# Kernel tuning notes

Hardware: AMD Instinct MI355X
Metric: run time of the kernel (lower is better)

## Reference

```python
import jax, jax.numpy as jnp
import numpy as np

FACTOR = 1  # init factor -> top_k = int(factor * log(L))


def setup_inputs() -> dict:
    key = jax.random.key(0)
    kq, kk, kv = jax.random.split(key, 3)
    B, L, H, E = 16, 2048, 8, 64
    shape = (B, L, H, E)
    return {
        "queries": jax.random.normal(kq, shape, dtype=jnp.float32),
        "keys": jax.random.normal(kk, shape, dtype=jnp.float32),
        "values": jax.random.normal(kv, shape, dtype=jnp.float32),
    }


def reference(queries, keys, values):
    B, L, H, E = queries.shape
    # seq lens equal -> torch's pad/truncate branch is a no-op slice
    q = jnp.transpose(queries, (0, 2, 3, 1))  # [B,H,E,L]
    k = jnp.transpose(keys, (0, 2, 3, 1))
    v = jnp.transpose(values, (0, 2, 3, 1))

    # FFT-based circular cross-correlation along time
    qf = jnp.fft.rfft(q, axis=-1)
    kf = jnp.fft.rfft(k, axis=-1)
    corr = jnp.fft.irfft(qf * jnp.conj(kf), n=L, axis=-1)  # [B,H,E,L]

    top_k = int(FACTOR * np.log(L))  # static: 7 for L=2048
    mean_value = corr.mean(axis=(1, 2))  # mean over head then variates -> [B,L]
    # global (batch-averaged) top-k delays, shared across batch (training path)
    _, topk_index = jax.lax.top_k(mean_value.mean(axis=0), top_k)  # [k]
    # per-batch weights at those delays, softmax over k
    w = jax.nn.softmax(mean_value[:, topk_index], axis=-1)  # [B,k]

    # torch.roll(v, -d, -1)[..., t] == v[..., (t + d) % L]
    idx = (jnp.arange(L)[None, :] + topk_index[:, None]) % L  # [k,L]
    gathered = v[..., idx]  # [B,H,E,k,L]
    agg = jnp.einsum('bhekl,bk->bhel', gathered, w)  # weighted delay aggregation

    return jnp.transpose(agg, (0, 3, 1, 2))  # back to [B,L,H,E]
```

## Files before the change

kernel.cpp:

```cpp
#include <hip/hip_runtime.h>
#include <hip/hip_bf16.h>
#include <math.h>


#define B_ 16
#define L_ 2048
#define H_ 8
#define E_ 64
#define C_ (H_ * E_)
#define NCH (B_ * C_)
#define K_ 7

#define PART_OFF 0ull
#define SG_OFF   33554432ull
#define MV_OFF   (SG_OFF + 2097152ull)
#define TK_OFF   (MV_OFF + 131072ull)
#define W_OFF    (TK_OFF + 64ull)

__device__ __forceinline__ float2 cadd(float2 a, float2 b) { return make_float2(a.x + b.x, a.y + b.y); }
__device__ __forceinline__ float2 csub(float2 a, float2 b) { return make_float2(a.x - b.x, a.y - b.y); }
__device__ __forceinline__ float2 cmul(float2 a, float2 b) {
  return make_float2(fmaf(a.x, b.x, -a.y * b.y), fmaf(a.x, b.y, a.y * b.x));
}
__device__ __forceinline__ float2 cis(float ang) { float s, c; sincosf(ang, &s, &c); return make_float2(c, s); }

template<int S> __device__ __forceinline__ float2 rot90(float2 z) {
  return (S < 0) ? make_float2(z.y, -z.x) : make_float2(-z.y, z.x);
}
template<int S> __device__ __forceinline__ void dft4(float2& a, float2& b, float2& c, float2& d) {
  float2 t0 = cadd(a, c), t1 = csub(a, c), t2 = cadd(b, d), t3 = rot90<S>(csub(b, d));
  a = cadd(t0, t2); c = csub(t0, t2); b = cadd(t1, t3); d = csub(t1, t3);
}
template<int S> __device__ __forceinline__ void dft8(float2 v[8]) {
  const float RT = 0.70710678118654752f;
  const float SR = (S < 0) ? -RT : RT;
  float2 a0 = cadd(v[0], v[4]), a1 = cadd(v[1], v[5]), a2 = cadd(v[2], v[6]), a3 = cadd(v[3], v[7]);
  float2 b0 = csub(v[0], v[4]), b1 = csub(v[1], v[5]), b2 = csub(v[2], v[6]), b3 = csub(v[3], v[7]);
  b1 = cmul(b1, make_float2(RT, SR));
  b2 = rot90<S>(b2);
  b3 = cmul(b3, make_float2(-RT, SR));
  dft4<S>(a0, a1, a2, a3);
  dft4<S>(b0, b1, b2, b3);
  v[0] = a0; v[2] = a1; v[4] = a2; v[6] = a3;
  v[1] = b0; v[3] = b1; v[5] = b2; v[7] = b3;
}
__device__ __forceinline__ int sg(int e) { return e + (e >> 5); }

__global__ __launch_bounds__(256) void fft_corr_kernel(
    const float* __restrict__ q, const float* __restrict__ k,
    float2* __restrict__ part) {
  extern __shared__ float2 dbuf[];
  int t = threadIdx.x;
  int j2 = t & 31, j3 = t & 3;
  float2 tw1[7], tw2[7], tw3[7];
  {
    float2 w1 = cis(-6.283185307179586f * (float)t  / 2048.0f);
    float2 w2 = cis(-6.283185307179586f * (float)j2 / 256.0f);
    float2 w3 = cis(-6.283185307179586f * (float)j3 / 32.0f);
    tw1[0] = w1; tw2[0] = w2; tw3[0] = w3;
#pragma unroll
    for (int kk = 1; kk < 7; ++kk) {
      tw1[kk] = cmul(tw1[kk - 1], w1);
      tw2[kk] = cmul(tw2[kk - 1], w2);
      tw3[kk] = cmul(tw3[kk - 1], w3);
    }
  }
  int pphys = blockIdx.x;
  int i = pphys >> 3, x = pphys & 7;
  int l = ((i >> 2) << 5) | (x << 2) | (i & 3);
  int cbase = l * 4;
  int b = cbase >> 9, h = (cbase >> 6) & 7, e0 = cbase & 63;
  size_t base = (size_t)b * (L_ * H_ * E_) + (size_t)h * E_ + e0;

  float4 qv[8], kv[8];
#pragma unroll
  for (int m = 0; m < 8; ++m) {
    size_t a = base + (size_t)(t + 256 * m) * (H_ * E_);
    qv[m] = *(const float4*)(q + a);
    kv[m] = *(const float4*)(k + a);
  }

  float2 acc[8];
#pragma unroll
  for (int kk = 0; kk < 8; ++kk) acc[kk] = make_float2(0.f, 0.f);

#pragma unroll
  for (int c = 0; c < 4; ++c) {
    float2 v[8];
#pragma unroll
    for (int m = 0; m < 8; ++m)
      v[m] = make_float2(((const float*)&qv[m])[c], ((const float*)&kv[m])[c]);
    dft8<-1>(v);
#pragma unroll
    for (int kk = 1; kk < 8; ++kk) v[kk] = cmul(v[kk], tw1[kk - 1]);
    float2* bufc = dbuf + c * 2112;
#pragma unroll
    for (int kk = 0; kk < 8; ++kk) bufc[sg(t + 256 * kk)] = v[kk];
  }
  __syncthreads();

  int base2 = (t >> 5) * 256 + j2;
  int base3 = (t >> 2) * 32 + j3;
#pragma unroll
  for (int cp = 0; cp < 2; ++cp) {
    float2* A  = dbuf + (2 * cp) * 2112;
    float2* Bf = dbuf + (2 * cp + 1) * 2112;
    float2 va[8], vb[8];
#pragma unroll
    for (int m = 0; m < 8; ++m) { va[m] = A[sg(base2 + 32 * m)]; vb[m] = Bf[sg(base2 + 32 * m)]; }
    dft8<-1>(va); dft8<-1>(vb);
#pragma unroll
    for (int kk = 1; kk < 8; ++kk) { va[kk] = cmul(va[kk], tw2[kk - 1]); vb[kk] = cmul(vb[kk], tw2[kk - 1]); }
#pragma unroll
    for (int kk = 0; kk < 8; ++kk) { A[sg(base2 + 32 * kk)] = va[kk]; Bf[sg(base2 + 32 * kk)] = vb[kk]; }
    __syncthreads();
#pragma unroll
    for (int m = 0; m < 8; ++m) { va[m] = A[sg(base3 + 4 * m)]; vb[m] = Bf[sg(base3 + 4 * m)]; }
    dft8<-1>(va); dft8<-1>(vb);
#pragma unroll
    for (int kk = 1; kk < 8; ++kk) { va[kk] = cmul(va[kk], tw3[kk - 1]); vb[kk] = cmul(vb[kk], tw3[kk - 1]); }
#pragma unroll
    for (int kk = 0; kk < 8; ++kk) { A[sg(base3 + 4 * kk)] = va[kk]; Bf[sg(base3 + 4 * kk)] = vb[kk]; }
    __syncthreads();
#pragma unroll
    for (int kk = 0; kk < 8; ++kk) { va[kk] = A[sg(8 * t + kk)]; vb[kk] = Bf[sg(8 * t + kk)]; }
    dft4<-1>(va[0], va[1], va[2], va[3]); dft4<-1>(va[4], va[5], va[6], va[7]);
    dft4<-1>(vb[0], vb[1], vb[2], vb[3]); dft4<-1>(vb[4], vb[5], vb[6], vb[7]);
#pragma unroll
    for (int kk = 0; kk < 8; ++kk) { A[sg(8 * t + kk)] = va[kk]; Bf[sg(8 * t + kk)] = vb[kk]; }
    __syncthreads();
#pragma unroll
    for (int kk = 0; kk < 8; ++kk) {
      int pos = 8 * t + kk;
      int f  = ((pos >> 8) & 7) | (((pos >> 5) & 7) << 3) | (((pos >> 2) & 7) << 6) | ((pos & 3) << 9);
      int fp = (2048 - f) & 2047;
      int pp = ((fp & 7) << 8) | (((fp >> 3) & 7) << 5) | (((fp >> 6) & 7) << 2) | ((fp >> 9) & 3);
      float2 Ax = va[kk], Bc = A[sg(pp)];
      acc[kk].x += 0.5f  * (Bc.x * Ax.y + Bc.y * Ax.x);
      acc[kk].y += 0.25f * (Ax.x * Ax.x + Ax.y * Ax.y - Bc.x * Bc.x - Bc.y * Bc.y);
      Ax = vb[kk]; Bc = Bf[sg(pp)];
      acc[kk].x += 0.5f  * (Bc.x * Ax.y + Bc.y * Ax.x);
      acc[kk].y += 0.25f * (Ax.x * Ax.x + Ax.y * Ax.y - Bc.x * Bc.x - Bc.y * Bc.y);
    }
  }
#pragma unroll
  for (int kk = 0; kk < 8; ++kk) dbuf[sg(8 * t + kk)] = acc[kk];
  __syncthreads();
  float2* prow = part + (size_t)l * L_;
#pragma unroll
  for (int m = 0; m < 8; ++m) prow[t + 256 * m] = dbuf[sg(t + 256 * m)];
}

__global__ __launch_bounds__(256) void reduce_R_kernel(
    const float2* __restrict__ part, float2* __restrict__ Sg) {
  int idx = blockIdx.x * 256 + threadIdx.x;
  int p = idx & 2047;
  int g = (idx >> 11) & 7;
  int b = idx >> 14;
  float2 s = make_float2(0.f, 0.f);
#pragma unroll 4
  for (int i = 0; i < 16; ++i) {
    float2 vv = part[(size_t)(b * 128 + g * 16 + i) * L_ + p];
    s.x += vv.x; s.y += vv.y;
  }
  Sg[idx] = s;
}

__global__ __launch_bounds__(256) void ifft_kernel(
    const float2* __restrict__ Sg, float* __restrict__ mv) {
  __shared__ float2 buf[2112];
  int t = threadIdx.x, b = blockIdx.x;
  int j2 = t & 31, j3 = t & 3;
  float2 tw1[7], tw2[7], tw3[7];
  {
    float2 w1 = cis(6.283185307179586f * (float)t  / 2048.0f);
    float2 w2 = cis(6.283185307179586f * (float)j2 / 256.0f);
    float2 w3 = cis(6.283185307179586f * (float)j3 / 32.0f);
    tw1[0] = w1; tw2[0] = w2; tw3[0] = w3;
#pragma unroll
    for (int kk = 1; kk < 7; ++kk) {
      tw1[kk] = cmul(tw1[kk - 1], w1);
      tw2[kk] = cmul(tw2[kk - 1], w2);
      tw3[kk] = cmul(tw3[kk - 1], w3);
    }
  }
  int base2 = (t >> 5) * 256 + j2;
  int base3 = (t >> 2) * 32 + j3;
  float2 u[8];
#pragma unroll
  for (int kk = 0; kk < 8; ++kk) u[kk] = make_float2(0.f, 0.f);
#pragma unroll
  for (int g = 0; g < 8; ++g) {
    const float4* rp = (const float4*)(Sg + (size_t)(b * 8 + g) * L_);
#pragma unroll
    for (int m = 0; m < 4; ++m) {
      float4 f = rp[4 * t + m];
      u[2 * m].x     += f.x; u[2 * m].y     += f.y;
      u[2 * m + 1].x += f.z; u[2 * m + 1].y += f.w;
    }
  }
  dft4<1>(u[0], u[1], u[2], u[3]);
  dft4<1>(u[4], u[5], u[6], u[7]);
#pragma unroll
  for (int kk = 0; kk < 8; ++kk) buf[sg(8 * t + kk)] = u[kk];
  __syncthreads();
  float2 v[8];
#pragma unroll
  for (int kk = 0; kk < 8; ++kk) v[kk] = buf[sg(base3 + 4 * kk)];
#pragma unroll
  for (int kk = 1; kk < 8; ++kk) v[kk] = cmul(v[kk], tw3[kk - 1]);
  dft8<1>(v);
  __syncthreads();
#pragma unroll
  for (int m = 0; m < 8; ++m) buf[sg(base3 + 4 * m)] = v[m];
  __syncthreads();
#pragma unroll
  for (int kk = 0; kk < 8; ++kk) v[kk] = buf[sg(base2 + 32 * kk)];
#pragma unroll
  for (int kk = 1; kk < 8; ++kk) v[kk] = cmul(v[kk], tw2[kk - 1]);
  dft8<1>(v);
  __syncthreads();
#pragma unroll
  for (int m = 0; m < 8; ++m) buf[sg(base2 + 32 * m)] = v[m];
  __syncthreads();
#pragma unroll
  for (int kk = 0; kk < 8; ++kk) v[kk] = buf[sg(t + 256 * kk)];
#pragma unroll
  for (int kk = 1; kk < 8; ++kk) v[kk] = cmul(v[kk], tw1[kk - 1]);
  dft8<1>(v);
  const float scale = 1.0f / (2048.0f * 512.0f);
#pragma unroll
  for (int m = 0; m < 8; ++m) mv[b * L_ + t + 256 * m] = v[m].x * scale;
}

__global__ __launch_bounds__(256) void topk_kernel(
    const float* __restrict__ mv, int* __restrict__ topk, float* __restrict__ wts) {
  __shared__ float av[2048];
  __shared__ float rv[256];
  __shared__ int   ri[256];
  __shared__ int   sidx[K_];
  int tid = threadIdx.x;
  for (int d = tid; d < 2048; d += 256) {
    float s = 0.f;
#pragma unroll
    for (int b = 0; b < B_; ++b) s += mv[b * L_ + d];
    av[d] = s;
  }
  __syncthreads();
  for (int kk = 0; kk < K_; ++kk) {
    float bv = -INFINITY; int bi = 0;
    for (int d = tid; d < 2048; d += 256) {
      float vv = av[d];
      if (vv > bv) { bv = vv; bi = d; }
    }
    rv[tid] = bv; ri[tid] = bi;
    __syncthreads();
    for (int off = 128; off > 0; off >>= 1) {
      if (tid < off) {
        float v2 = rv[tid + off]; int i2 = ri[tid + off];
        if (v2 > rv[tid] || (v2 == rv[tid] && i2 < ri[tid])) { rv[tid] = v2; ri[tid] = i2; }
      }
      __syncthreads();
    }
    if (tid == 0) { sidx[kk] = ri[0]; av[ri[0]] = -INFINITY; }
    __syncthreads();
  }
  if (tid < K_) topk[tid] = sidx[tid];
  if (tid < B_) {
    float xk[K_], m = -INFINITY;
#pragma unroll
    for (int kk = 0; kk < K_; ++kk) { xk[kk] = mv[tid * L_ + sidx[kk]]; m = fmaxf(m, xk[kk]); }
    float s = 0.f;
#pragma unroll
    for (int kk = 0; kk < K_; ++kk) { xk[kk] = expf(xk[kk] - m); s += xk[kk]; }
#pragma unroll
    for (int kk = 0; kk < K_; ++kk) wts[tid * K_ + kk] = xk[kk] / s;
  }
}

__global__ __launch_bounds__(256) void aggregate_kernel(
    const float4* __restrict__ v4, const int* __restrict__ topk,
    const float* __restrict__ wts, float4* __restrict__ out4) {
  __shared__ int   sidx[K_];
  __shared__ float sw[B_][K_];
  int tid = threadIdx.x;
  if (tid < K_) sidx[tid] = topk[tid];
  if (tid < B_ * K_) sw[tid / K_][tid % K_] = wts[tid];
  __syncthreads();
  int idx = blockIdx.x * 256 + tid;
  int c4  = idx & 127;
  int row = idx >> 7;
  int t   = row & (L_ - 1);
  int b   = row >> 11;
  float4 acc = make_float4(0.f, 0.f, 0.f, 0.f);
#pragma unroll
  for (int kk = 0; kk < K_; ++kk) {
    int s = t + sidx[kk];
    if (s >= L_) s -= L_;
    float w = sw[b][kk];
    float4 val = v4[((size_t)(b * L_ + s) << 7) + c4];
    acc.x += w * val.x; acc.y += w * val.y;
    acc.z += w * val.z; acc.w += w * val.w;
  }
  out4[idx] = acc;
}

extern "C" void kernel_launch(void* const* d_in, const int* in_sizes, int n_in,
                              void* d_out, int out_size, void* d_ws, size_t ws_size,
                              hipStream_t stream) {
  const float* q = (const float*)d_in[0];
  const float* k = (const float*)d_in[1];
  const float* v = (const float*)d_in[2];
  float* out = (float*)d_out;

  char* ws = (char*)d_ws;
  float2* part = (float2*)(ws + PART_OFF);
  float2* Sg   = (float2*)(ws + SG_OFF);
  float*  mv   = (float*) (ws + MV_OFF);
  int*    topk = (int*)   (ws + TK_OFF);
  float*  wts  = (float*) (ws + W_OFF);

  fft_corr_kernel<<<NCH / 4, 256, 4 * 2112 * sizeof(float2), stream>>>(q, k, part);
  reduce_R_kernel<<<(B_ * 8 * L_) / 256, 256, 0, stream>>>(part, Sg);
  ifft_kernel<<<B_, 256, 0, stream>>>(Sg, mv);
  topk_kernel<<<1, 256, 0, stream>>>(mv, topk, wts);
  aggregate_kernel<<<(B_ * L_ * C_ / 4) / 256, 256, 0, stream>>>(
      (const float4*)v, topk, wts, (float4*)out);
}
```

Before: 156.9 us.

## Process two channels per FFT block instead of four to cut LDS and registers

The FFT correlation kernel now handles 2 channels per block (float2 loads) instead of 4, halving shared memory per block and register usage, and doubling the block count. The partial-sum buffer grows to twice as many rows, so the reduce kernel sums 32 partials instead of 16 and the workspace offset moves. The LDS padding changes from one slot per 32 to one per 16 elements to reduce bank conflicts. In exchange, global loads are narrower, twice as much partial data is written and re-read, and twiddle setup is repeated across twice as many blocks.

```diff
diff --git a/kernel.cpp b/kernel.cpp
--- a/kernel.cpp
+++ b/kernel.cpp
@@ -9,10 +9,12 @@
 #define E_ 64
 #define C_ (H_ * E_)
 #define NCH (B_ * C_)
+#define NBLK (NCH / 2)
 #define K_ 7
+#define PAD_ 2176
 
 #define PART_OFF 0ull
-#define SG_OFF   33554432ull
+#define SG_OFF   67108864ull
 #define MV_OFF   (SG_OFF + 2097152ull)
 #define TK_OFF   (MV_OFF + 131072ull)
 #define W_OFF    (TK_OFF + 64ull)
@@ -44,7 +46,7 @@
   v[0] = a0; v[2] = a1; v[4] = a2; v[6] = a3;
   v[1] = b0; v[3] = b1; v[5] = b2; v[7] = b3;
 }
-__device__ __forceinline__ int sg(int e) { return e + (e >> 5); }
+__device__ __forceinline__ int sg(int e) { return e + (e >> 4); }
 
 __global__ __launch_bounds__(256) void fft_corr_kernel(
     const float* __restrict__ q, const float* __restrict__ k,
@@ -67,82 +69,82 @@
   }
   int pphys = blockIdx.x;
   int i = pphys >> 3, x = pphys & 7;
-  int l = ((i >> 2) << 5) | (x << 2) | (i & 3);
-  int cbase = l * 4;
+  int l = ((((i >> 3) << 3) | x) << 3) | (i & 7);
+  int cbase = l * 2;
   int b = cbase >> 9, h = (cbase >> 6) & 7, e0 = cbase & 63;
   size_t base = (size_t)b * (L_ * H_ * E_) + (size_t)h * E_ + e0;
 
-  float4 qv[8], kv[8];
+  float2 qv[8], kv[8];
 #pragma unroll
   for (int m = 0; m < 8; ++m) {
     size_t a = base + (size_t)(t + 256 * m) * (H_ * E_);
-    qv[m] = *(const float4*)(q + a);
-    kv[m] = *(const float4*)(k + a);
-  }
-
-  float2 acc[8];
-#pragma unroll
-  for (int kk = 0; kk < 8; ++kk) acc[kk] = make_float2(0.f, 0.f);
-
-#pragma unroll
-  for (int c = 0; c < 4; ++c) {
+    qv[m] = *(const float2*)(q + a);
+    kv[m] = *(const float2*)(k + a);
+  }
+
+  float2* A  = dbuf;
+  float2* Bf = dbuf + PAD_;
+
+  {
     float2 v[8];
 #pragma unroll
-    for (int m = 0; m < 8; ++m)
-      v[m] = make_float2(((const float*)&qv[m])[c], ((const float*)&kv[m])[c]);
+    for (int m = 0; m < 8; ++m) v[m] = make_float2(qv[m].x, kv[m].x);
     dft8<-1>(v);
 #pragma unroll
     for (int kk = 1; kk < 8; ++kk) v[kk] = cmul(v[kk], tw1[kk - 1]);
-    float2* bufc = dbuf + c * 2112;
-#pragma unroll
-    for (int kk = 0; kk < 8; ++kk) bufc[sg(t + 256 * kk)] = v[kk];
+#pragma unroll
+    for (int kk = 0; kk < 8; ++kk) A[sg(t + 256 * kk)] = v[kk];
+#pragma unroll
+    for (int m = 0; m < 8; ++m) v[m] = make_float2(qv[m].y, kv[m].y);
+    dft8<-1>(v);
+#pragma unroll
+    for (int kk = 1; kk < 8; ++kk) v[kk] = cmul(v[kk], tw1[kk - 1]);
+#pragma unroll
+    for (int kk = 0; kk < 8; ++kk) Bf[sg(t + 256 * kk)] = v[kk];
   }
   __syncthreads();
 
   int base2 = (t >> 5) * 256 + j2;
   int base3 = (t >> 2) * 32 + j3;
-#pragma unroll
-  for (int cp = 0; cp < 2; ++cp) {
-    float2* A  = dbuf + (2 * cp) * 2112;
-    float2* Bf = dbuf + (2 * cp + 1) * 2112;
-    float2 va[8], vb[8];
-#pragma unroll
-    for (int m = 0; m < 8; ++m) { va[m] = A[sg(base2 + 32 * m)]; vb[m] = Bf[sg(base2 + 32 * m)]; }
-    dft8<-1>(va); dft8<-1>(vb);
-#pragma unroll
-    for (int kk = 1; kk < 8; ++kk) { va[kk] = cmul(va[kk], tw2[kk - 1]); vb[kk] = cmul(vb[kk], tw2[kk - 1]); }
-#pragma unroll
-    for (int kk = 0; kk < 8; ++kk) { A[sg(base2 + 32 * kk)] = va[kk]; Bf[sg(base2 + 32 * kk)] = vb[kk]; }
-    __syncthreads();
-#pragma unroll
-    for (int m = 0; m < 8; ++m) { va[m] = A[sg(base3 + 4 * m)]; vb[m] = Bf[sg(base3 + 4 * m)]; }
-    dft8<-1>(va); dft8<-1>(vb);
-#pragma unroll
-    for (int kk = 1; kk < 8; ++kk) { va[kk] = cmul(va[kk], tw3[kk - 1]); vb[kk] = cmul(vb[kk], tw3[kk - 1]); }
-#pragma unroll
-    for (int kk = 0; kk < 8; ++kk) { A[sg(base3 + 4 * kk)] = va[kk]; Bf[sg(base3 + 4 * kk)] = vb[kk]; }
-    __syncthreads();
-#pragma unroll
-    for (int kk = 0; kk < 8; ++kk) { va[kk] = A[sg(8 * t + kk)]; vb[kk] = Bf[sg(8 * t + kk)]; }
-    dft4<-1>(va[0], va[1], va[2], va[3]); dft4<-1>(va[4], va[5], va[6], va[7]);
-    dft4<-1>(vb[0], vb[1], vb[2], vb[3]); dft4<-1>(vb[4], vb[5], vb[6], vb[7]);
-#pragma unroll
-    for (int kk = 0; kk < 8; ++kk) { A[sg(8 * t + kk)] = va[kk]; Bf[sg(8 * t + kk)] = vb[kk]; }
-    __syncthreads();
-#pragma unroll
-    for (int kk = 0; kk < 8; ++kk) {
-      int pos = 8 * t + kk;
-      int f  = ((pos >> 8) & 7) | (((pos >> 5) & 7) << 3) | (((pos >> 2) & 7) << 6) | ((pos & 3) << 9);
-      int fp = (2048 - f) & 2047;
-      int pp = ((fp & 7) << 8) | (((fp >> 3) & 7) << 5) | (((fp >> 6) & 7) << 2) | ((fp >> 9) & 3);
-      float2 Ax = va[kk], Bc = A[sg(pp)];
-      acc[kk].x += 0.5f  * (Bc.x * Ax.y + Bc.y * Ax.x);
-      acc[kk].y += 0.25f * (Ax.x * Ax.x + Ax.y * Ax.y - Bc.x * Bc.x - Bc.y * Bc.y);
-      Ax = vb[kk]; Bc = Bf[sg(pp)];
-      acc[kk].x += 0.5f  * (Bc.x * Ax.y + Bc.y * Ax.x);
-      acc[kk].y += 0.25f * (Ax.x * Ax.x + Ax.y * Ax.y - Bc.x * Bc.x - Bc.y * Bc.y);
-    }
-  }
+  float2 va[8], vb[8];
+#pragma unroll
+  for (int m = 0; m < 8; ++m) { va[m] = A[sg(base2 + 32 * m)]; vb[m] = Bf[sg(base2 + 32 * m)]; }
+  dft8<-1>(va); dft8<-1>(vb);
+#pragma unroll
+  for (int kk = 1; kk < 8; ++kk) { va[kk] = cmul(va[kk], tw2[kk - 1]); vb[kk] = cmul(vb[kk], tw2[kk - 1]); }
+#pragma unroll
+  for (int kk = 0; kk < 8; ++kk) { A[sg(base2 + 32 * kk)] = va[kk]; Bf[sg(base2 + 32 * kk)] = vb[kk]; }
+  __syncthreads();
+#pragma unroll
+  for (int m = 0; m < 8; ++m) { va[m] = A[sg(base3 + 4 * m)]; vb[m] = Bf[sg(base3 + 4 * m)]; }
+  dft8<-1>(va); dft8<-1>(vb);
+#pragma unroll
+  for (int kk = 1; kk < 8; ++kk) { va[kk] = cmul(va[kk], tw3[kk - 1]); vb[kk] = cmul(vb[kk], tw3[kk - 1]); }
+#pragma unroll
+  for (int kk = 0; kk < 8; ++kk) { A[sg(base3 + 4 * kk)] = va[kk]; Bf[sg(base3 + 4 * kk)] = vb[kk]; }
+  __syncthreads();
+#pragma unroll
+  for (int kk = 0; kk < 8; ++kk) { va[kk] = A[sg(8 * t + kk)]; vb[kk] = Bf[sg(8 * t + kk)]; }
+  dft4<-1>(va[0], va[1], va[2], va[3]); dft4<-1>(va[4], va[5], va[6], va[7]);
+  dft4<-1>(vb[0], vb[1], vb[2], vb[3]); dft4<-1>(vb[4], vb[5], vb[6], vb[7]);
+#pragma unroll
+  for (int kk = 0; kk < 8; ++kk) { A[sg(8 * t + kk)] = va[kk]; Bf[sg(8 * t + kk)] = vb[kk]; }
+  __syncthreads();
+  float2 acc[8];
+#pragma unroll
+  for (int kk = 0; kk < 8; ++kk) {
+    int pos = 8 * t + kk;
+    int f  = ((pos >> 8) & 7) | (((pos >> 5) & 7) << 3) | (((pos >> 2) & 7) << 6) | ((pos & 3) << 9);
+    int fp = (2048 - f) & 2047;
+    int pp = ((fp & 7) << 8) | (((fp >> 3) & 7) << 5) | (((fp >> 6) & 7) << 2) | ((fp >> 9) & 3);
+    float2 Ax = va[kk], Bc = A[sg(pp)];
+    acc[kk].x = 0.5f  * (Bc.x * Ax.y + Bc.y * Ax.x);
+    acc[kk].y = 0.25f * (Ax.x * Ax.x + Ax.y * Ax.y - Bc.x * Bc.x - Bc.y * Bc.y);
+    Ax = vb[kk]; Bc = Bf[sg(pp)];
+    acc[kk].x += 0.5f  * (Bc.x * Ax.y + Bc.y * Ax.x);
+    acc[kk].y += 0.25f * (Ax.x * Ax.x + Ax.y * Ax.y - Bc.x * Bc.x - Bc.y * Bc.y);
+  }
+  __syncthreads();
 #pragma unroll
   for (int kk = 0; kk < 8; ++kk) dbuf[sg(8 * t + kk)] = acc[kk];
   __syncthreads();
@@ -159,8 +161,8 @@
   int b = idx >> 14;
   float2 s = make_float2(0.f, 0.f);
 #pragma unroll 4
-  for (int i = 0; i < 16; ++i) {
-    float2 vv = part[(size_t)(b * 128 + g * 16 + i) * L_ + p];
+  for (int i = 0; i < 32; ++i) {
+    float2 vv = part[(size_t)(b * 256 + g * 32 + i) * L_ + p];
     s.x += vv.x; s.y += vv.y;
   }
   Sg[idx] = s;
@@ -168,7 +170,7 @@
 
 __global__ __launch_bounds__(256) void ifft_kernel(
     const float2* __restrict__ Sg, float* __restrict__ mv) {
-  __shared__ float2 buf[2112];
+  __shared__ float2 buf[PAD_];
   int t = threadIdx.x, b = blockIdx.x;
   int j2 = t & 31, j3 = t & 3;
   float2 tw1[7], tw2[7], tw3[7];
@@ -320,7 +322,7 @@
   int*    topk = (int*)   (ws + TK_OFF);
   float*  wts  = (float*) (ws + W_OFF);
 
-  fft_corr_kernel<<<NCH / 4, 256, 4 * 2112 * sizeof(float2), stream>>>(q, k, part);
+  fft_corr_kernel<<<NBLK, 256, 2 * PAD_ * sizeof(float2), stream>>>(q, k, part);
   reduce_R_kernel<<<(B_ * 8 * L_) / 256, 256, 0, stream>>>(part, Sg);
   ifft_kernel<<<B_, 256, 0, stream>>>(Sg, mv);
   topk_kernel<<<1, 256, 0, stream>>>(mv, topk, wts);
```

Result: slower. 229.3 us (+46.2%).

## Process 16 channels per block with fp16 shared FFT buffers and drop reduce kernel

Applied to the files above, without the earlier changes.

Each FFT block now handles 16 channels with 512 threads and stages q/k in shared memory as half2, so the whole block's working set fits. Partial spectra are summed in-block and written as one row per block, removing the separate reduce kernel; the ifft kernel sums 32 rows per batch directly. The aim is to cut global partial traffic and one launch, at the cost of fp16 rounding inside the FFT stages, which may perturb top-k selection.

```diff
diff --git a/kernel.cpp b/kernel.cpp
--- a/kernel.cpp
+++ b/kernel.cpp
@@ -1,5 +1,6 @@
 #include <hip/hip_runtime.h>
 #include <hip/hip_bf16.h>
+#include <hip/hip_fp16.h>
 #include <math.h>
 
 
@@ -7,13 +8,12 @@
 #define L_ 2048
 #define H_ 8
 #define E_ 64
-#define C_ (H_ * E_)
-#define NCH (B_ * C_)
+#define NBLK 512
 #define K_ 7
+#define RS_ 2178
 
 #define PART_OFF 0ull
-#define SG_OFF   33554432ull
-#define MV_OFF   (SG_OFF + 2097152ull)
+#define MV_OFF   8388608ull
 #define TK_OFF   (MV_OFF + 131072ull)
 #define W_OFF    (TK_OFF + 64ull)
 
@@ -44,14 +44,40 @@
   v[0] = a0; v[2] = a1; v[4] = a2; v[6] = a3;
   v[1] = b0; v[3] = b1; v[5] = b2; v[7] = b3;
 }
-__device__ __forceinline__ int sg(int e) { return e + (e >> 5); }
-
-__global__ __launch_bounds__(256) void fft_corr_kernel(
+__device__ __forceinline__ int sg(int e) { return e + (e >> 4); }
+
+__device__ __forceinline__ float2 ld16(const __half2* p) { return __half22float2(*p); }
+__device__ __forceinline__ void st16(__half2* p, float2 v) { *p = __float22half2_rn(v); }
+
+__global__ __launch_bounds__(512) void fft_corr_kernel(
     const float* __restrict__ q, const float* __restrict__ k,
     float2* __restrict__ part) {
-  extern __shared__ float2 dbuf[];
-  int t = threadIdx.x;
+  extern __shared__ __half2 dbuf[];
+  int tid = threadIdx.x;
+  int t = tid & 255;
+  int half = tid >> 8;
   int j2 = t & 31, j3 = t & 3;
+  int l = blockIdx.x;
+  int eg = l & 3, h = (l >> 2) & 7, b = l >> 5;
+  size_t base = (size_t)b * (L_ * H_ * E_) + (size_t)h * E_ + eg * 16;
+
+  {
+    int f4 = tid & 3, tau0 = tid >> 2;
+#pragma unroll 4
+    for (int m = 0; m < 16; ++m) {
+      int tau = tau0 + 128 * m;
+      size_t a = base + (size_t)tau * (H_ * E_) + f4 * 4;
+      float4 q4 = *(const float4*)(q + a);
+      float4 k4 = *(const float4*)(k + a);
+      int sp = sg(tau);
+      st16(&dbuf[(4 * f4 + 0) * RS_ + sp], make_float2(q4.x, k4.x));
+      st16(&dbuf[(4 * f4 + 1) * RS_ + sp], make_float2(q4.y, k4.y));
+      st16(&dbuf[(4 * f4 + 2) * RS_ + sp], make_float2(q4.z, k4.z));
+      st16(&dbuf[(4 * f4 + 3) * RS_ + sp], make_float2(q4.w, k4.w));
+    }
+  }
+  __syncthreads();
+
   float2 tw1[7], tw2[7], tw3[7];
   {
     float2 w1 = cis(-6.283185307179586f * (float)t  / 2048.0f);
@@ -65,69 +91,46 @@
       tw3[kk] = cmul(tw3[kk - 1], w3);
     }
   }
-  int pphys = blockIdx.x;
-  int i = pphys >> 3, x = pphys & 7;
-  int l = ((i >> 2) << 5) | (x << 2) | (i & 3);
-  int cbase = l * 4;
-  int b = cbase >> 9, h = (cbase >> 6) & 7, e0 = cbase & 63;
-  size_t base = (size_t)b * (L_ * H_ * E_) + (size_t)h * E_ + e0;
-
-  float4 qv[8], kv[8];
-#pragma unroll
-  for (int m = 0; m < 8; ++m) {
-    size_t a = base + (size_t)(t + 256 * m) * (H_ * E_);
-    qv[m] = *(const float4*)(q + a);
-    kv[m] = *(const float4*)(k + a);
-  }
-
-  float2 acc[8];
-#pragma unroll
-  for (int kk = 0; kk < 8; ++kk) acc[kk] = make_float2(0.f, 0.f);
-
-#pragma unroll
-  for (int c = 0; c < 4; ++c) {
-    float2 v[8];
-#pragma unroll
-    for (int m = 0; m < 8; ++m)
-      v[m] = make_float2(((const float*)&qv[m])[c], ((const float*)&kv[m])[c]);
-    dft8<-1>(v);
-#pragma unroll
-    for (int kk = 1; kk < 8; ++kk) v[kk] = cmul(v[kk], tw1[kk - 1]);
-    float2* bufc = dbuf + c * 2112;
-#pragma unroll
-    for (int kk = 0; kk < 8; ++kk) bufc[sg(t + 256 * kk)] = v[kk];
-  }
-  __syncthreads();
-
   int base2 = (t >> 5) * 256 + j2;
   int base3 = (t >> 2) * 32 + j3;
-#pragma unroll
-  for (int cp = 0; cp < 2; ++cp) {
-    float2* A  = dbuf + (2 * cp) * 2112;
-    float2* Bf = dbuf + (2 * cp + 1) * 2112;
+  float2 acc[8];
+#pragma unroll
+  for (int kk = 0; kk < 8; ++kk) acc[kk] = make_float2(0.f, 0.f);
+
+  for (int p = 0; p < 4; ++p) {
+    __half2* A  = dbuf + (size_t)(4 * p + 2 * half) * RS_;
+    __half2* Bf = A + RS_;
     float2 va[8], vb[8];
 #pragma unroll
-    for (int m = 0; m < 8; ++m) { va[m] = A[sg(base2 + 32 * m)]; vb[m] = Bf[sg(base2 + 32 * m)]; }
+    for (int m = 0; m < 8; ++m) { va[m] = ld16(&A[sg(t + 256 * m)]); vb[m] = ld16(&Bf[sg(t + 256 * m)]); }
     dft8<-1>(va); dft8<-1>(vb);
 #pragma unroll
+    for (int kk = 1; kk < 8; ++kk) { va[kk] = cmul(va[kk], tw1[kk - 1]); vb[kk] = cmul(vb[kk], tw1[kk - 1]); }
+#pragma unroll
+    for (int kk = 0; kk < 8; ++kk) { st16(&A[sg(t + 256 * kk)], va[kk]); st16(&Bf[sg(t + 256 * kk)], vb[kk]); }
+    __syncthreads();
+#pragma unroll
+    for (int m = 0; m < 8; ++m) { va[m] = ld16(&A[sg(base2 + 32 * m)]); vb[m] = ld16(&Bf[sg(base2 + 32 * m)]); }
+    dft8<-1>(va); dft8<-1>(vb);
+#pragma unroll
     for (int kk = 1; kk < 8; ++kk) { va[kk] = cmul(va[kk], tw2[kk - 1]); vb[kk] = cmul(vb[kk], tw2[kk - 1]); }
 #pragma unroll
-    for (int kk = 0; kk < 8; ++kk) { A[sg(base2 + 32 * kk)] = va[kk]; Bf[sg(base2 + 32 * kk)] = vb[kk]; }
-    __syncthreads();
-#pragma unroll
-    for (int m = 0; m < 8; ++m) { va[m] = A[sg(base3 + 4 * m)]; vb[m] = Bf[sg(base3 + 4 * m)]; }
+    for (int kk = 0; kk < 8; ++kk) { st16(&A[sg(base2 + 32 * kk)], va[kk]); st16(&Bf[sg(base2 + 32 * kk)], vb[kk]); }
+    __syncthreads();
+#pragma unroll
+    for (int m = 0; m < 8; ++m) { va[m] = ld16(&A[sg(base3 + 4 * m)]); vb[m] = ld16(&Bf[sg(base3 + 4 * m)]); }
     dft8<-1>(va); dft8<-1>(vb);
 #pragma unroll
     for (int kk = 1; kk < 8; ++kk) { va[kk] = cmul(va[kk], tw3[kk - 1]); vb[kk] = cmul(vb[kk], tw3[kk - 1]); }
 #pragma unroll
-    for (int kk = 0; kk < 8; ++kk) { A[sg(base3 + 4 * kk)] = va[kk]; Bf[sg(base3 + 4 * kk)] = vb[kk]; }
-    __syncthreads();
-#pragma unroll
-    for (int kk = 0; kk < 8; ++kk) { va[kk] = A[sg(8 * t + kk)]; vb[kk] = Bf[sg(8 * t + kk)]; }
+    for (int kk = 0; kk < 8; ++kk) { st16(&A[sg(base3 + 4 * kk)], va[kk]); st16(&Bf[sg(base3 + 4 * kk)], vb[kk]); }
+    __syncthreads();
+#pragma unroll
+    for (int kk = 0; kk < 8; ++kk) { va[kk] = ld16(&A[sg(8 * t + kk)]); vb[kk] = ld16(&Bf[sg(8 * t + kk)]); }
     dft4<-1>(va[0], va[1], va[2], va[3]); dft4<-1>(va[4], va[5], va[6], va[7]);
     dft4<-1>(vb[0], vb[1], vb[2], vb[3]); dft4<-1>(vb[4], vb[5], vb[6], vb[7]);
 #pragma unroll
-    for (int kk = 0; kk < 8; ++kk) { A[sg(8 * t + kk)] = va[kk]; Bf[sg(8 * t + kk)] = vb[kk]; }
+    for (int kk = 0; kk < 8; ++kk) { st16(&A[sg(8 * t + kk)], va[kk]); st16(&Bf[sg(8 * t + kk)], vb[kk]); }
     __syncthreads();
 #pragma unroll
     for (int kk = 0; kk < 8; ++kk) {
@@ -135,40 +138,43 @@
       int f  = ((pos >> 8) & 7) | (((pos >> 5) & 7) << 3) | (((pos >> 2) & 7) << 6) | ((pos & 3) << 9);
       int fp = (2048 - f) & 2047;
       int pp = ((fp & 7) << 8) | (((fp >> 3) & 7) << 5) | (((fp >> 6) & 7) << 2) | ((fp >> 9) & 3);
-      float2 Ax = va[kk], Bc = A[sg(pp)];
+      float2 Ax = va[kk], Bc = ld16(&A[sg(pp)]);
       acc[kk].x += 0.5f  * (Bc.x * Ax.y + Bc.y * Ax.x);
       acc[kk].y += 0.25f * (Ax.x * Ax.x + Ax.y * Ax.y - Bc.x * Bc.x - Bc.y * Bc.y);
-      Ax = vb[kk]; Bc = Bf[sg(pp)];
+      Ax = vb[kk]; Bc = ld16(&Bf[sg(pp)]);
       acc[kk].x += 0.5f  * (Bc.x * Ax.y + Bc.y * Ax.x);
       acc[kk].y += 0.25f * (Ax.x * Ax.x + Ax.y * Ax.y - Bc.x * Bc.x - Bc.y * Bc.y);
     }
   }
-#pragma unroll
-  for (int kk = 0; kk < 8; ++kk) dbuf[sg(8 * t + kk)] = acc[kk];
-  __syncthreads();
-  float2* prow = part + (size_t)l * L_;
-#pragma unroll
-  for (int m = 0; m < 8; ++m) prow[t + 256 * m] = dbuf[sg(t + 256 * m)];
-}
-
-__global__ __launch_bounds__(256) void reduce_R_kernel(
-    const float2* __restrict__ part, float2* __restrict__ Sg) {
-  int idx = blockIdx.x * 256 + threadIdx.x;
-  int p = idx & 2047;
-  int g = (idx >> 11) & 7;
-  int b = idx >> 14;
-  float2 s = make_float2(0.f, 0.f);
-#pragma unroll 4
-  for (int i = 0; i < 16; ++i) {
-    float2 vv = part[(size_t)(b * 128 + g * 16 + i) * L_ + p];
-    s.x += vv.x; s.y += vv.y;
-  }
-  Sg[idx] = s;
+  {
+    float* fre = (float*)dbuf + (size_t)(2 * half) * RS_;
+    float* fim = fre + RS_;
+#pragma unroll
+    for (int kk = 0; kk < 8; ++kk) {
+      int sp = sg(8 * t + kk);
+      fre[sp] = acc[kk].x;
+      fim[sp] = acc[kk].y;
+    }
+  }
+  __syncthreads();
+  {
+    const float* r0 = (const float*)dbuf;
+    const float* i0 = r0 + RS_;
+    const float* r1 = r0 + 2 * RS_;
+    const float* i1 = r0 + 3 * RS_;
+    float2* prow = part + (size_t)l * L_;
+#pragma unroll
+    for (int m = 0; m < 4; ++m) {
+      int p = tid + 512 * m;
+      int sp = sg(p);
+      prow[p] = make_float2(r0[sp] + r1[sp], i0[sp] + i1[sp]);
+    }
+  }
 }
 
 __global__ __launch_bounds__(256) void ifft_kernel(
-    const float2* __restrict__ Sg, float* __restrict__ mv) {
-  __shared__ float2 buf[2112];
+    const float2* __restrict__ part, float* __restrict__ mv) {
+  __shared__ float2 buf[2176];
   int t = threadIdx.x, b = blockIdx.x;
   int j2 = t & 31, j3 = t & 3;
   float2 tw1[7], tw2[7], tw3[7];
@@ -189,9 +195,9 @@
   float2 u[8];
 #pragma unroll
   for (int kk = 0; kk < 8; ++kk) u[kk] = make_float2(0.f, 0.f);
-#pragma unroll
-  for (int g = 0; g < 8; ++g) {
-    const float4* rp = (const float4*)(Sg + (size_t)(b * 8 + g) * L_);
+#pragma unroll 4
+  for (int g = 0; g < 32; ++g) {
+    const float4* rp = (const float4*)(part + (size_t)(b * 32 + g) * L_);
 #pragma unroll
     for (int m = 0; m < 4; ++m) {
       float4 f = rp[4 * t + m];
@@ -315,15 +321,13 @@
 
   char* ws = (char*)d_ws;
   float2* part = (float2*)(ws + PART_OFF);
-  float2* Sg   = (float2*)(ws + SG_OFF);
   float*  mv   = (float*) (ws + MV_OFF);
   int*    topk = (int*)   (ws + TK_OFF);
   float*  wts  = (float*) (ws + W_OFF);
 
-  fft_corr_kernel<<<NCH / 4, 256, 4 * 2112 * sizeof(float2), stream>>>(q, k, part);
-  reduce_R_kernel<<<(B_ * 8 * L_) / 256, 256, 0, stream>>>(part, Sg);
-  ifft_kernel<<<B_, 256, 0, stream>>>(Sg, mv);
+  fft_corr_kernel<<<NBLK, 512, 16 * RS_ * 4, stream>>>(q, k, part);
+  ifft_kernel<<<B_, 256, 0, stream>>>(part, mv);
   topk_kernel<<<1, 256, 0, stream>>>(mv, topk, wts);
-  aggregate_kernel<<<(B_ * L_ * C_ / 4) / 256, 256, 0, stream>>>(
+  aggregate_kernel<<<(B_ * L_ * H_ * E_ / 4) / 256, 256, 0, stream>>>(
       (const float4*)v, topk, wts, (float4*)out);
 }
```

After: 159.6 us. About the same (+1.7%).
